# Kernel tuning notes

Hardware: AMD Instinct MI355X
Metric: run time of the kernel (lower is better)

The kernel has to match this reference:

```python
import jax, jax.numpy as jnp
import numpy as np

EMBED_DIM = 1024
NUM_HEADS = 16
HEAD_DIM = EMBED_DIM // NUM_HEADS
ROPE_BASE = 10000.0


def setup_inputs() -> dict:
    key = jax.random.key(0)
    ks = jax.random.split(key, 5)
    B, S, E = 4, 2048, EMBED_DIM
    hidden = jax.random.normal(ks[0], (B, S, E), dtype=jnp.float32)
    sc_in = 1.0 / np.sqrt(E)
    qkv_w = jax.random.normal(ks[1], (3 * E, E), dtype=jnp.float32) * sc_in
    qkv_b = jnp.zeros((3 * E,), dtype=jnp.float32)
    proj_w = jax.random.normal(ks[2], (E, E), dtype=jnp.float32) * sc_in
    proj_b = jnp.zeros((E,), dtype=jnp.float32)
    return {"hidden": hidden, "qkv_w": qkv_w, "qkv_b": qkv_b,
            "proj_w": proj_w, "proj_b": proj_b}


def _rope_cos_sin(position_ids, head_dim, base):
    # position_ids: [B, S] int; returns cos/sin of shape [B, 1, S, head_dim]
    inv_freq = 1.0 / (base ** (jnp.arange(0, head_dim, 2, dtype=jnp.float32) / head_dim))
    freqs = position_ids.astype(jnp.float32)[..., None] * inv_freq  # [B,S,hd/2]
    emb = jnp.concatenate([freqs, freqs], axis=-1)                  # [B,S,hd]
    return jnp.cos(emb)[:, None], jnp.sin(emb)[:, None]


def _rotate_half(x):
    x1, x2 = jnp.split(x, 2, axis=-1)
    return jnp.concatenate([-x2, x1], axis=-1)


def reference(hidden, qkv_w, qkv_b, proj_w, proj_b):
    B, S, E = hidden.shape
    H, hd = NUM_HEADS, HEAD_DIM
    qkv = hidden @ qkv_w.T + qkv_b                    # [B,S,3E]
    qkv = qkv.reshape(B, S, 3, H, hd).transpose(2, 0, 3, 1, 4)  # [3,B,H,S,hd]
    q, k, v = qkv[0], qkv[1], qkv[2]
    pos = jnp.broadcast_to(jnp.arange(S)[None, :], (B, S))
    cos, sin = _rope_cos_sin(pos, hd, ROPE_BASE)      # [B,1,S,hd]
    q = q * cos + _rotate_half(q) * sin
    k = k * cos + _rotate_half(k) * sin
    scale = 1.0 / jnp.sqrt(jnp.float32(hd))
    scores = jnp.einsum("bhsd,bhtd->bhst", q, k) * scale
    attn = jax.nn.softmax(scores, axis=-1)
    out = jnp.einsum("bhst,bhtd->bhsd", attn, v)      # [B,H,S,hd]
    out = out.transpose(0, 2, 1, 3).reshape(B, S, E)
    return out @ proj_w.T + proj_b
```

## Files before the change

kernel.cpp:

```cpp
#include <hip/hip_runtime.h>
#include <cstdint>
#include <cstddef>

typedef _Float16 f16;
typedef __attribute__((ext_vector_type(4))) float f32x4;
typedef __attribute__((ext_vector_type(8))) _Float16 f16x8;
typedef __attribute__((ext_vector_type(4))) _Float16 f16x4;

#define S_SEQ 2048
#define E_DIM 1024

#define OFF_HID   0ull
#define OFF_QKVW  8388608ull
#define OFF_PROJW 11534336ull
#define OFF_Q     12582912ull
#define OFF_K     20971520ull
#define OFF_VT    29360128ull
#define OFF_AO    37748736ull

__device__ __forceinline__ void async_copy16(const void* g, void* l) {
  __builtin_amdgcn_global_load_lds(
      (const __attribute__((address_space(1))) unsigned int*)g,
      (__attribute__((address_space(3))) unsigned int*)l, 16, 0, 0);
}

__device__ __forceinline__ float fast_exp2(float x) {
#if __has_builtin(__builtin_amdgcn_exp2f)
  return __builtin_amdgcn_exp2f(x);
#else
  return __expf(x * 0.6931471805599453f);
#endif
}

__global__ __launch_bounds__(256) void cvt_kernel(const float* __restrict__ hid,
                                                  const float* __restrict__ qw,
                                                  const float* __restrict__ pw,
                                                  f16* __restrict__ ws) {
  long i = (long)blockIdx.x * 256 + threadIdx.x;
  const float* src;
  f16* dst;
  long idx;
  if (i < 2097152L) { src = hid; dst = ws + OFF_HID;  idx = i; }
  else if (i < 2883584L) { src = qw; dst = ws + OFF_QKVW; idx = i - 2097152L; }
  else { src = pw; dst = ws + OFF_PROJW; idx = i - 2883584L; }
  float4 v = *(const float4*)(src + idx * 4);
  f16x4 o = { (f16)v.x, (f16)v.y, (f16)v.z, (f16)v.w };
  *(f16x4*)(dst + idx * 4) = o;
}

template <int MODE>
__global__ __launch_bounds__(256)
void gemm_kernel(const f16* __restrict__ A, const f16* __restrict__ Bm,
                 const float* __restrict__ bias,
                 f16* __restrict__ q_out, f16* __restrict__ k_out,
                 f16* __restrict__ vT_out, float* __restrict__ f_out) {
  __shared__ __align__(16) f16 As[2][128 * 32];
  __shared__ __align__(16) f16 Bs[2][128 * 32];
  const int tid = threadIdx.x;
  const int wave = tid >> 6;
  const int lane = tid & 63;
  const int q4 = lane >> 4;
  const int l16 = lane & 15;
  const int m0 = blockIdx.y * 128;
  const int n0 = blockIdx.x * 128;
  const int wr = (wave >> 1) * 64;
  const int wc = (wave & 1) * 64;
  f32x4 acc[4][4] = {};

  const int srow = tid >> 2;
  const int scol = (tid & 3) * 8;

  auto stage = [&](int k0, int b) {
    for (int p = 0; p < 2; ++p) {
      int row = p * 64 + srow;
      async_copy16(A + (size_t)(m0 + row) * 1024 + k0 + scol,
                   &As[b][(size_t)(p * 256 + wave * 64) * 8]);
      async_copy16(Bm + (size_t)(n0 + row) * 1024 + k0 + scol,
                   &Bs[b][(size_t)(p * 256 + wave * 64) * 8]);
    }
  };

  stage(0, 0);
  __syncthreads();
  int buf = 0;
  for (int k0 = 0; k0 < 1024; k0 += 32) {
    if (k0 + 32 < 1024) stage(k0 + 32, buf ^ 1);
    f16x8 af[4], bf[4];
    for (int mt = 0; mt < 4; ++mt)
      af[mt] = *(const f16x8*)&As[buf][(wr + mt * 16 + l16) * 32 + q4 * 8];
    for (int nt = 0; nt < 4; ++nt)
      bf[nt] = *(const f16x8*)&Bs[buf][(wc + nt * 16 + l16) * 32 + q4 * 8];
    for (int mt = 0; mt < 4; ++mt)
      for (int nt = 0; nt < 4; ++nt)
        acc[mt][nt] = __builtin_amdgcn_mfma_f32_16x16x32_f16(af[mt], bf[nt],
                                                             acc[mt][nt], 0, 0, 0);
    __syncthreads();
    buf ^= 1;
  }

  if constexpr (MODE == 0) {
    const int bx = blockIdx.x;
    const int part = bx >> 3;
    const int h = (((bx & 7) * 128) + wc) >> 6;
    float bv[4];
    for (int nt = 0; nt < 4; ++nt) bv[nt] = bias[n0 + wc + nt * 16 + l16];
    if (part < 2) {
      f16* outp = (part == 0) ? q_out : k_out;
      const float qscale = (part == 0) ? 0.18033688011112042f : 1.0f;
      float invf[2];
      for (int nt = 0; nt < 2; ++nt)
        invf[nt] = __expf(-(float)(nt * 16 + l16) * 0.2878231366242557f);
      for (int mt = 0; mt < 4; ++mt) {
        int mbase = m0 + wr + mt * 16 + q4 * 4;
        for (int r = 0; r < 4; ++r) {
          int mm = mbase + r;
          int b = mm >> 11, s = mm & 2047;
          size_t rowb = ((size_t)((b * 16 + h) * 2048 + s)) * 64;
          for (int nt = 0; nt < 2; ++nt) {
            float x1 = acc[mt][nt][r] + bv[nt];
            float x2 = acc[mt][nt + 2][r] + bv[nt + 2];
            float ang = (float)s * invf[nt];
            float sn, cs;
            __sincosf(ang, &sn, &cs);
            float o1 = (x1 * cs - x2 * sn) * qscale;
            float o2 = (x2 * cs + x1 * sn) * qscale;
            int d1 = nt * 16 + l16;
            outp[rowb + d1] = (f16)o1;
            outp[rowb + d1 + 32] = (f16)o2;
          }
        }
      }
    } else {
      for (int mt = 0; mt < 4; ++mt) {
        int mbase = m0 + wr + mt * 16 + q4 * 4;
        int b = mbase >> 11, s0 = mbase & 2047;
        for (int nt = 0; nt < 4; ++nt) {
          int d = nt * 16 + l16;
          size_t basei = ((size_t)((b * 16 + h) * 64 + d)) * 2048 + s0;
          f16x4 pk;
          for (int r = 0; r < 4; ++r) pk[r] = (f16)(acc[mt][nt][r] + bv[nt]);
          *(f16x4*)&vT_out[basei] = pk;
        }
      }
    }
  } else {
    float bv[4];
    for (int nt = 0; nt < 4; ++nt) bv[nt] = bias[n0 + wc + nt * 16 + l16];
    for (int mt = 0; mt < 4; ++mt)
      for (int r = 0; r < 4; ++r) {
        int mm = m0 + wr + mt * 16 + q4 * 4 + r;
        for (int nt = 0; nt < 4; ++nt)
          f_out[(size_t)mm * 1024 + n0 + wc + nt * 16 + l16] = acc[mt][nt][r] + bv[nt];
      }
  }
}

__global__ __launch_bounds__(256, 2)
void attn_kernel(const f16* __restrict__ Qg, const f16* __restrict__ Kg,
                 const f16* __restrict__ VTg, f16* __restrict__ AOg) {
  __shared__ __align__(16) f16 smem[2][8704];
  const int tid = threadIdx.x;
  const int wave = tid >> 6, lane = tid & 63;
  const int q4 = lane >> 4, l16 = lane & 15;
  const int qt = blockIdx.x, bh = blockIdx.y;
  const f16* Qb = Qg + (size_t)bh * (S_SEQ * 64);
  const f16* Kb = Kg + (size_t)bh * (S_SEQ * 64);
  const f16* Vb = VTg + (size_t)bh * (64 * S_SEQ);
  const int ws0 = wave * 64;

  f16x8 qf[4][2];
#pragma unroll
  for (int sn = 0; sn < 4; ++sn)
#pragma unroll
    for (int kf = 0; kf < 2; ++kf)
      qf[sn][kf] = *(const f16x8*)(Qb + (size_t)(qt * 256 + ws0 + sn * 16 + l16) * 64
                                      + kf * 32 + q4 * 8);

  f32x4 o[4][4] = {};
  f32x4 lacc[4] = {};
  f16x8 ones;
#pragma unroll
  for (int j = 0; j < 8; ++j) ones[j] = (f16)1.0f;

  const int srow = tid >> 3;
  const int scol = (tid & 7) * 8;

  const int kcs = scol >> 5;
  const int hs8 = ((scol >> 4) & 1) * 8;
  const int q0s = (scol & 15) >> 2;
  const int slot0 = kcs * 4 + q0s;
  const int swzA = (((slot0) ^ (srow & 7)) << 4) + hs8;
  const int swzB = (((slot0 + 1) ^ (srow & 7)) << 4) + hs8;

  int4 k0r = *(const int4*)(Kb + (size_t)srow * 64 + scol);
  int4 k1r = *(const int4*)(Kb + (size_t)(32 + srow) * 64 + scol);
  f16x8 v0r = *(const f16x8*)(Vb + (size_t)srow * 2048 + scol);
  f16x8 v1r = *(const f16x8*)(Vb + (size_t)(32 + srow) * 2048 + scol);
  {
    f16* Kn = smem[0];
    char* Vn = (char*)(smem[0] + 4608);
    *(int4*)(Kn + srow * 72 + scol) = k0r;
    *(int4*)(Kn + (32 + srow) * 72 + scol) = k1r;
    f16x4 lo0 = {v0r[0], v0r[1], v0r[2], v0r[3]};
    f16x4 hi0 = {v0r[4], v0r[5], v0r[6], v0r[7]};
    f16x4 lo1 = {v1r[0], v1r[1], v1r[2], v1r[3]};
    f16x4 hi1 = {v1r[4], v1r[5], v1r[6], v1r[7]};
    *(f16x4*)(Vn + srow * 128 + swzA) = lo0;
    *(f16x4*)(Vn + srow * 128 + swzB) = hi0;
    *(f16x4*)(Vn + (32 + srow) * 128 + swzA) = lo1;
    *(f16x4*)(Vn + (32 + srow) * 128 + swzB) = hi1;
  }
  __syncthreads();

  int cur = 0;
  for (int tt = 0; tt < 32; ++tt) {
    const f16* Kc = smem[cur];
    const char* Vc = (const char*)(smem[cur] + 4608);

    if (tt + 1 < 32) {
      const int t0n = (tt + 1) * 64;
      k0r = *(const int4*)(Kb + (size_t)(t0n + srow) * 64 + scol);
      k1r = *(const int4*)(Kb + (size_t)(t0n + 32 + srow) * 64 + scol);
      v0r = *(const f16x8*)(Vb + (size_t)srow * 2048 + t0n + scol);
      v1r = *(const f16x8*)(Vb + (size_t)(32 + srow) * 2048 + t0n + scol);
    }

    f16x8 kf0[4], kf1[4];
#pragma unroll
    for (int tm = 0; tm < 4; ++tm) {
      kf0[tm] = *(const f16x8*)(Kc + (tm * 16 + l16) * 72 + q4 * 8);
      kf1[tm] = *(const f16x8*)(Kc + (tm * 16 + l16) * 72 + 32 + q4 * 8);
    }
    f16x8 vf[4][2];
#pragma unroll
    for (int dm = 0; dm < 4; ++dm)
#pragma unroll
      for (int kc = 0; kc < 2; ++kc)
        vf[dm][kc] = *(const f16x8*)(Vc + (dm * 16 + l16) * 128 +
                                     (((kc * 4 + q4) ^ (l16 & 7)) << 4));

#pragma unroll
    for (int sn = 0; sn < 4; ++sn) {
      f32x4 st[4];
#pragma unroll
      for (int tm = 0; tm < 4; ++tm) {
        f32x4 c = {0.f, 0.f, 0.f, 0.f};
        c = __builtin_amdgcn_mfma_f32_16x16x32_f16(kf0[tm], qf[sn][0], c, 0, 0, 0);
        c = __builtin_amdgcn_mfma_f32_16x16x32_f16(kf1[tm], qf[sn][1], c, 0, 0, 0);
        st[tm] = c;
      }
#pragma unroll
      for (int tm = 0; tm < 4; ++tm)
#pragma unroll
        for (int r = 0; r < 4; ++r)
          st[tm][r] = fast_exp2(st[tm][r]);
#pragma unroll
      for (int kc = 0; kc < 2; ++kc) {
        f16x8 pf;
        pf[0] = (f16)st[kc * 2][0];
        pf[1] = (f16)st[kc * 2][1];
        pf[2] = (f16)st[kc * 2][2];
        pf[3] = (f16)st[kc * 2][3];
        pf[4] = (f16)st[kc * 2 + 1][0];
        pf[5] = (f16)st[kc * 2 + 1][1];
        pf[6] = (f16)st[kc * 2 + 1][2];
        pf[7] = (f16)st[kc * 2 + 1][3];
        lacc[sn] = __builtin_amdgcn_mfma_f32_16x16x32_f16(ones, pf, lacc[sn], 0, 0, 0);
#pragma unroll
        for (int dm = 0; dm < 4; ++dm)
          o[dm][sn] = __builtin_amdgcn_mfma_f32_16x16x32_f16(vf[dm][kc], pf,
                                                             o[dm][sn], 0, 0, 0);
      }
    }

    if (tt + 1 < 32) {
      f16* Kn = smem[cur ^ 1];
      char* Vn = (char*)(smem[cur ^ 1] + 4608);
      *(int4*)(Kn + srow * 72 + scol) = k0r;
      *(int4*)(Kn + (32 + srow) * 72 + scol) = k1r;
      f16x4 lo0 = {v0r[0], v0r[1], v0r[2], v0r[3]};
      f16x4 hi0 = {v0r[4], v0r[5], v0r[6], v0r[7]};
      f16x4 lo1 = {v1r[0], v1r[1], v1r[2], v1r[3]};
      f16x4 hi1 = {v1r[4], v1r[5], v1r[6], v1r[7]};
      *(f16x4*)(Vn + srow * 128 + swzA) = lo0;
      *(f16x4*)(Vn + srow * 128 + swzB) = hi0;
      *(f16x4*)(Vn + (32 + srow) * 128 + swzA) = lo1;
      *(f16x4*)(Vn + (32 + srow) * 128 + swzB) = hi1;
    }
    __syncthreads();
    cur ^= 1;
  }

  float inv_l[4];
#pragma unroll
  for (int sn = 0; sn < 4; ++sn) inv_l[sn] = 1.0f / lacc[sn][0];
  f16* Ot = smem[0];
#pragma unroll
  for (int sn = 0; sn < 4; ++sn) {
    int so = ws0 + sn * 16 + l16;
#pragma unroll
    for (int dm = 0; dm < 4; ++dm) {
      f16x4 w;
      w[0] = (f16)(o[dm][sn][0] * inv_l[sn]);
      w[1] = (f16)(o[dm][sn][1] * inv_l[sn]);
      w[2] = (f16)(o[dm][sn][2] * inv_l[sn]);
      w[3] = (f16)(o[dm][sn][3] * inv_l[sn]);
      *(f16x4*)(Ot + so * 64 + dm * 16 + q4 * 4) = w;
    }
  }
  __syncthreads();
  const int b = bh >> 4, h = bh & 15;
#pragma unroll
  for (int half = 0; half < 2; ++half) {
    const int sr = half * 128 + (tid >> 1), dh = (tid & 1) * 32;
    size_t gbase = ((size_t)(b * 2048 + qt * 256 + sr)) * 1024 + h * 64 + dh;
#pragma unroll
    for (int c = 0; c < 4; ++c) {
      f16x8 v = *(const f16x8*)(Ot + sr * 64 + dh + c * 8);
      *(f16x8*)(AOg + gbase + c * 8) = v;
    }
  }
}

extern "C" void kernel_launch(void* const* d_in, const int* in_sizes, int n_in,
                              void* d_out, int out_size, void* d_ws, size_t ws_size,
                              hipStream_t stream) {
  const float* hid   = (const float*)d_in[0];
  const float* qkvw  = (const float*)d_in[1];
  const float* qkvb  = (const float*)d_in[2];
  const float* projw = (const float*)d_in[3];
  const float* projb = (const float*)d_in[4];
  float* out = (float*)d_out;
  f16* ws = (f16*)d_ws;

  cvt_kernel<<<12288, 256, 0, stream>>>(hid, qkvw, projw, ws);
  gemm_kernel<0><<<dim3(24, 64), 256, 0, stream>>>(
      ws + OFF_HID, ws + OFF_QKVW, qkvb,
      ws + OFF_Q, ws + OFF_K, ws + OFF_VT, nullptr);
  attn_kernel<<<dim3(8, 64), 256, 0, stream>>>(
      ws + OFF_Q, ws + OFF_K, ws + OFF_VT, ws + OFF_AO);
  gemm_kernel<1><<<dim3(8, 64), 256, 0, stream>>>(
      ws + OFF_AO, ws + OFF_PROJW, projb,
      nullptr, nullptr, nullptr, out);
}
```

Before: 269.0 us.

## Triple-buffer GEMM LDS staging with XOR swizzle and explicit vmcnt waits

Moves the shared QKV/projection GEMM main loop from double to triple buffering, keeping two async global-to-LDS stages in flight and waiting with explicit vmcnt counts and raw s_barrier in place of __syncthreads. It also applies an XOR swizzle to the LDS column layout, both where data is written and where fragments are read, to cut bank conflicts on the f16x8 fragment loads. The intent is to hide global load latency behind MFMA work and reduce LDS stalls. The cost is 50% more LDS per block, which may lower occupancy, and more fragile hand-written synchronisation.

```diff
diff --git a/kernel.cpp b/kernel.cpp
--- a/kernel.cpp
+++ b/kernel.cpp
@@ -54,8 +54,8 @@
                  const float* __restrict__ bias,
                  f16* __restrict__ q_out, f16* __restrict__ k_out,
                  f16* __restrict__ vT_out, float* __restrict__ f_out) {
-  __shared__ __align__(16) f16 As[2][128 * 32];
-  __shared__ __align__(16) f16 Bs[2][128 * 32];
+  __shared__ __align__(16) f16 As[3][128 * 32];
+  __shared__ __align__(16) f16 Bs[3][128 * 32];
   const int tid = threadIdx.x;
   const int wave = tid >> 6;
   const int lane = tid & 63;
@@ -68,7 +68,7 @@
   f32x4 acc[4][4] = {};
 
   const int srow = tid >> 2;
-  const int scol = (tid & 3) * 8;
+  const int scol = (((tid & 3) ^ ((srow >> 2) & 3)) * 8);
 
   auto stage = [&](int k0, int b) {
     for (int p = 0; p < 2; ++p) {
@@ -80,23 +80,63 @@
     }
   };
 
+#define GEMM_STEP(cb, sb, ks, DO_STAGE, VMN)                                 \
+  {                                                                          \
+    if (DO_STAGE) stage(((ks) + 2) * 32, sb);                                \
+    f16x8 af[4], bf[4];                                                      \
+    _Pragma("unroll")                                                        \
+    for (int mt = 0; mt < 4; ++mt) {                                         \
+      int row = wr + mt * 16 + l16;                                          \
+      af[mt] = *(const f16x8*)&As[cb][row * 32 + (q4 ^ ((row >> 2) & 3)) * 8]; \
+    }                                                                        \
+    _Pragma("unroll")                                                        \
+    for (int nt = 0; nt < 4; ++nt) {                                         \
+      int row = wc + nt * 16 + l16;                                          \
+      bf[nt] = *(const f16x8*)&Bs[cb][row * 32 + (q4 ^ ((row >> 2) & 3)) * 8]; \
+    }                                                                        \
+    asm volatile("s_waitcnt lgkmcnt(0)" ::: "memory");                       \
+    __builtin_amdgcn_sched_barrier(0);                                       \
+    _Pragma("unroll")                                                        \
+    for (int mt = 0; mt < 4; ++mt)                                           \
+      _Pragma("unroll")                                                      \
+      for (int nt = 0; nt < 4; ++nt)                                         \
+        acc[mt][nt] = __builtin_amdgcn_mfma_f32_16x16x32_f16(                \
+            af[mt], bf[nt], acc[mt][nt], 0, 0, 0);                           \
+    asm volatile("s_waitcnt vmcnt(" #VMN ")" ::: "memory");                  \
+    __builtin_amdgcn_s_barrier();                                            \
+  }
+
   stage(0, 0);
-  __syncthreads();
-  int buf = 0;
-  for (int k0 = 0; k0 < 1024; k0 += 32) {
-    if (k0 + 32 < 1024) stage(k0 + 32, buf ^ 1);
+  stage(32, 1);
+  asm volatile("s_waitcnt vmcnt(4)" ::: "memory");
+  __builtin_amdgcn_s_barrier();
+
+  for (int k3 = 0; k3 < 30; k3 += 3) {
+    GEMM_STEP(0, 2, (k3 + 0), 1, 4);
+    GEMM_STEP(1, 0, (k3 + 1), 1, 4);
+    GEMM_STEP(2, 1, (k3 + 2), 1, 4);
+  }
+  GEMM_STEP(0, 0, 30, 0, 0);
+  {
     f16x8 af[4], bf[4];
+#pragma unroll
+    for (int mt = 0; mt < 4; ++mt) {
+      int row = wr + mt * 16 + l16;
+      af[mt] = *(const f16x8*)&As[1][row * 32 + (q4 ^ ((row >> 2) & 3)) * 8];
+    }
+#pragma unroll
+    for (int nt = 0; nt < 4; ++nt) {
+      int row = wc + nt * 16 + l16;
+      bf[nt] = *(const f16x8*)&Bs[1][row * 32 + (q4 ^ ((row >> 2) & 3)) * 8];
+    }
+#pragma unroll
     for (int mt = 0; mt < 4; ++mt)
-      af[mt] = *(const f16x8*)&As[buf][(wr + mt * 16 + l16) * 32 + q4 * 8];
-    for (int nt = 0; nt < 4; ++nt)
-      bf[nt] = *(const f16x8*)&Bs[buf][(wc + nt * 16 + l16) * 32 + q4 * 8];
-    for (int mt = 0; mt < 4; ++mt)
+#pragma unroll
       for (int nt = 0; nt < 4; ++nt)
         acc[mt][nt] = __builtin_amdgcn_mfma_f32_16x16x32_f16(af[mt], bf[nt],
                                                              acc[mt][nt], 0, 0, 0);
-    __syncthreads();
-    buf ^= 1;
-  }
+  }
+#undef GEMM_STEP
 
   if constexpr (MODE == 0) {
     const int bx = blockIdx.x;
```

After: 270.7 us. No clear change (+0.6%).

## Restructure GEMM main loop into split-K half phases with finer waitcnt pipelining

Applied to the files above, without the earlier changes.

The GEMM K-loop now works on 64-wide K tiles, each split into two 32-wide halves with their own double-buffered LDS slots. Each phase reads its fragments with inline ds_read_b128, issues the async global-to-LDS copy for the next tile's matching half, and waits on explicit vmcnt counters rather than draining all loads behind a full __syncthreads. MFMA bursts are wrapped in sched_barrier and s_setprio to keep them together and favour math issue. This aims to overlap global loads with compute more tightly, at the cost of doubled LDS use (lower occupancy) and fragile hand-managed waitcnt and barrier ordering.

```diff
diff --git a/kernel.cpp b/kernel.cpp
--- a/kernel.cpp
+++ b/kernel.cpp
@@ -22,6 +22,14 @@
   __builtin_amdgcn_global_load_lds(
       (const __attribute__((address_space(1))) unsigned int*)g,
       (__attribute__((address_space(3))) unsigned int*)l, 16, 0, 0);
+}
+
+__device__ __forceinline__ f16x8 lds_read_b128(const f16* p) {
+  f16x8 r;
+  const __attribute__((address_space(3))) f16* p3 =
+      (const __attribute__((address_space(3))) f16*)p;
+  asm volatile("ds_read_b128 %0, %1" : "=v"(r) : "v"(p3));
+  return r;
 }
 
 __device__ __forceinline__ float fast_exp2(float x) {
@@ -54,8 +62,8 @@
                  const float* __restrict__ bias,
                  f16* __restrict__ q_out, f16* __restrict__ k_out,
                  f16* __restrict__ vT_out, float* __restrict__ f_out) {
-  __shared__ __align__(16) f16 As[2][128 * 32];
-  __shared__ __align__(16) f16 Bs[2][128 * 32];
+  __shared__ __align__(16) f16 As[2][2][128 * 32];
+  __shared__ __align__(16) f16 Bs[2][2][128 * 32];
   const int tid = threadIdx.x;
   const int wave = tid >> 6;
   const int lane = tid & 63;
@@ -70,33 +78,54 @@
   const int srow = tid >> 2;
   const int scol = (tid & 3) * 8;
 
-  auto stage = [&](int k0, int b) {
-    for (int p = 0; p < 2; ++p) {
-      int row = p * 64 + srow;
-      async_copy16(A + (size_t)(m0 + row) * 1024 + k0 + scol,
-                   &As[b][(size_t)(p * 256 + wave * 64) * 8]);
-      async_copy16(Bm + (size_t)(n0 + row) * 1024 + k0 + scol,
-                   &Bs[b][(size_t)(p * 256 + wave * 64) * 8]);
-    }
+  auto stage = [&](int kt, int kh, int b) {
+    const f16* as = A + (size_t)(m0 + srow) * 1024 + kt * 64 + kh * 32 + scol;
+    async_copy16(as,             &As[b][kh][wave * 512]);
+    async_copy16(as + 64 * 1024, &As[b][kh][2048 + wave * 512]);
+    const f16* bs = Bm + (size_t)(n0 + srow) * 1024 + kt * 64 + kh * 32 + scol;
+    async_copy16(bs,             &Bs[b][kh][wave * 512]);
+    async_copy16(bs + 64 * 1024, &Bs[b][kh][2048 + wave * 512]);
   };
 
-  stage(0, 0);
-  __syncthreads();
-  int buf = 0;
-  for (int k0 = 0; k0 < 1024; k0 += 32) {
-    if (k0 + 32 < 1024) stage(k0 + 32, buf ^ 1);
-    f16x8 af[4], bf[4];
-    for (int mt = 0; mt < 4; ++mt)
-      af[mt] = *(const f16x8*)&As[buf][(wr + mt * 16 + l16) * 32 + q4 * 8];
-    for (int nt = 0; nt < 4; ++nt)
-      bf[nt] = *(const f16x8*)&Bs[buf][(wc + nt * 16 + l16) * 32 + q4 * 8];
-    for (int mt = 0; mt < 4; ++mt)
-      for (int nt = 0; nt < 4; ++nt)
-        acc[mt][nt] = __builtin_amdgcn_mfma_f32_16x16x32_f16(af[mt], bf[nt],
-                                                             acc[mt][nt], 0, 0, 0);
-    __syncthreads();
-    buf ^= 1;
-  }
+#define PHASE(T, KH, DO_STAGE, VMN)                                          \
+  {                                                                          \
+    const int cb_ = (T) & 1;                                                 \
+    f16x8 af[4], bf[4];                                                      \
+    _Pragma("unroll")                                                        \
+    for (int mt = 0; mt < 4; ++mt)                                           \
+      af[mt] = lds_read_b128(&As[cb_][KH][(wr + mt * 16 + l16) * 32 + q4 * 8]); \
+    _Pragma("unroll")                                                        \
+    for (int nt = 0; nt < 4; ++nt)                                           \
+      bf[nt] = lds_read_b128(&Bs[cb_][KH][(wc + nt * 16 + l16) * 32 + q4 * 8]); \
+    if (DO_STAGE) stage((T) + 1, KH, cb_ ^ 1);                               \
+    __builtin_amdgcn_s_barrier();                                            \
+    asm volatile("s_waitcnt lgkmcnt(0)" ::: "memory");                       \
+    __builtin_amdgcn_sched_barrier(0);                                       \
+    __builtin_amdgcn_s_setprio(1);                                           \
+    _Pragma("unroll")                                                        \
+    for (int mt = 0; mt < 4; ++mt)                                           \
+      _Pragma("unroll")                                                      \
+      for (int nt = 0; nt < 4; ++nt)                                         \
+        acc[mt][nt] = __builtin_amdgcn_mfma_f32_16x16x32_f16(                \
+            af[mt], bf[nt], acc[mt][nt], 0, 0, 0);                           \
+    __builtin_amdgcn_s_setprio(0);                                           \
+    __builtin_amdgcn_sched_barrier(0);                                       \
+    asm volatile("s_waitcnt vmcnt(" #VMN ")" ::: "memory");                  \
+    __builtin_amdgcn_s_barrier();                                            \
+  }
+
+  stage(0, 0, 0);
+  stage(0, 1, 0);
+  asm volatile("s_waitcnt vmcnt(4)" ::: "memory");
+  __builtin_amdgcn_s_barrier();
+
+  for (int t = 0; t < 15; ++t) {
+    PHASE(t, 0, 1, 4);
+    PHASE(t, 1, 1, 4);
+  }
+  PHASE(15, 0, 0, 0);
+  PHASE(15, 1, 0, 0);
+#undef PHASE
 
   if constexpr (MODE == 0) {
     const int bx = blockIdx.x;
```

New measurement: 268.1 us. About the same (-0.3%).

## Rewrite GEMM as 256x256 tile, 8-wave kernel with swizzled LDS and phased pipeline

Applied to the files above, without the earlier changes.

Rewrites the shared GEMM kernel so that 512 threads compute 256x256 output tiles with K-steps of 64. Global-to-LDS staging goes through XOR-swizzled async copies, and fragments are read with explicit ds_read_b128. The main loop is split into phases that interleave staging of the next tile with MFMA work under explicit barriers, waitcnt and setprio. The goal is more data reuse per loaded byte, fewer LDS bank conflicts and better overlap of loads with compute. In exchange the kernel needs much more register and LDS use, and the QKV GEMM launches only 384 blocks and the projection GEMM only 128, which can leave many of the chip's CUs idle.

```diff
diff --git a/kernel.cpp b/kernel.cpp
--- a/kernel.cpp
+++ b/kernel.cpp
@@ -22,6 +22,14 @@
   __builtin_amdgcn_global_load_lds(
       (const __attribute__((address_space(1))) unsigned int*)g,
       (__attribute__((address_space(3))) unsigned int*)l, 16, 0, 0);
+}
+
+__device__ __forceinline__ f16x8 lds_read_b128(const f16* p) {
+  f16x8 r;
+  const __attribute__((address_space(3))) f16* p3 =
+      (const __attribute__((address_space(3))) f16*)p;
+  asm volatile("ds_read_b128 %0, %1" : "=v"(r) : "v"(p3));
+  return r;
 }
 
 __device__ __forceinline__ float fast_exp2(float x) {
@@ -49,76 +57,129 @@
 }
 
 template <int MODE>
-__global__ __launch_bounds__(256)
+__global__ __launch_bounds__(512)
 void gemm_kernel(const f16* __restrict__ A, const f16* __restrict__ Bm,
                  const float* __restrict__ bias,
                  f16* __restrict__ q_out, f16* __restrict__ k_out,
                  f16* __restrict__ vT_out, float* __restrict__ f_out) {
-  __shared__ __align__(16) f16 As[2][128 * 32];
-  __shared__ __align__(16) f16 Bs[2][128 * 32];
+  __shared__ __align__(16) f16 As[2][2][8192];
+  __shared__ __align__(16) f16 Bs[2][2][8192];
   const int tid = threadIdx.x;
   const int wave = tid >> 6;
   const int lane = tid & 63;
   const int q4 = lane >> 4;
   const int l16 = lane & 15;
-  const int m0 = blockIdx.y * 128;
-  const int n0 = blockIdx.x * 128;
-  const int wr = (wave >> 1) * 64;
-  const int wc = (wave & 1) * 64;
-  f32x4 acc[4][4] = {};
-
-  const int srow = tid >> 2;
-  const int scol = (tid & 3) * 8;
-
-  auto stage = [&](int k0, int b) {
-    for (int p = 0; p < 2; ++p) {
-      int row = p * 64 + srow;
-      async_copy16(A + (size_t)(m0 + row) * 1024 + k0 + scol,
-                   &As[b][(size_t)(p * 256 + wave * 64) * 8]);
-      async_copy16(Bm + (size_t)(n0 + row) * 1024 + k0 + scol,
-                   &Bs[b][(size_t)(p * 256 + wave * 64) * 8]);
-    }
+  const int wm = wave >> 2;
+  const int wn = wave & 3;
+  const int m0 = blockIdx.y * 256;
+  const int n0 = blockIdx.x * 256;
+  f32x4 acc[8][4] = {};
+
+  const int gsl = ((lane & 3) ^ ((lane >> 2) & 3)) * 8;
+  const f16* Agp = A  + (size_t)(m0 + wave * 16 + (lane >> 2)) * 1024 + gsl;
+  const f16* Bgp = Bm + (size_t)(n0 + wave * 16 + (lane >> 2)) * 1024 + gsl;
+  char* AsW = (char*)&As[0][0][0] + wave * 1024;
+  char* BsW = (char*)&Bs[0][0][0] + wave * 1024;
+
+  auto stageA = [&](int kt, int kc, int sb) {
+    const f16* g = Agp + kt * 64 + kc * 32;
+    char* l = AsW + sb * 32768 + kc * 16384;
+    async_copy16(g, l);
+    async_copy16(g + 131072, l + 8192);
   };
-
-  stage(0, 0);
-  __syncthreads();
-  int buf = 0;
-  for (int k0 = 0; k0 < 1024; k0 += 32) {
-    if (k0 + 32 < 1024) stage(k0 + 32, buf ^ 1);
-    f16x8 af[4], bf[4];
-    for (int mt = 0; mt < 4; ++mt)
-      af[mt] = *(const f16x8*)&As[buf][(wr + mt * 16 + l16) * 32 + q4 * 8];
-    for (int nt = 0; nt < 4; ++nt)
-      bf[nt] = *(const f16x8*)&Bs[buf][(wc + nt * 16 + l16) * 32 + q4 * 8];
-    for (int mt = 0; mt < 4; ++mt)
-      for (int nt = 0; nt < 4; ++nt)
-        acc[mt][nt] = __builtin_amdgcn_mfma_f32_16x16x32_f16(af[mt], bf[nt],
-                                                             acc[mt][nt], 0, 0, 0);
-    __syncthreads();
-    buf ^= 1;
-  }
+  auto stageB = [&](int kt, int kc, int sb) {
+    const f16* g = Bgp + kt * 64 + kc * 32;
+    char* l = BsW + sb * 32768 + kc * 16384;
+    async_copy16(g, l);
+    async_copy16(g + 131072, l + 8192);
+  };
+
+  const int aoff = (wm * 128 + l16) * 32 + (q4 ^ (l16 & 3)) * 8;
+  const int boff = (wn * 64 + l16) * 32 + (q4 ^ (l16 & 3)) * 8;
+
+  f16x8 bf[4];
+
+#define PHASE(b_, kc_, mh_, STAGE_STMT, VM_STMT)                          \
+  do {                                                                    \
+    const f16* pA_ = &As[b_][kc_][0];                                     \
+    const f16* pB_ = &Bs[b_][kc_][0];                                     \
+    f16x8 af_[4];                                                         \
+    _Pragma("unroll")                                                     \
+    for (int i_ = 0; i_ < 4; ++i_)                                        \
+      af_[i_] = lds_read_b128(pA_ + aoff + (mh_) * 2048 + i_ * 512);      \
+    if ((mh_) == 0) {                                                     \
+      _Pragma("unroll")                                                   \
+      for (int nt_ = 0; nt_ < 4; ++nt_)                                   \
+        bf[nt_] = lds_read_b128(pB_ + boff + nt_ * 512);                  \
+    }                                                                     \
+    STAGE_STMT;                                                           \
+    __builtin_amdgcn_s_barrier();                                         \
+    asm volatile("s_waitcnt lgkmcnt(0)" ::: "memory");                    \
+    __builtin_amdgcn_sched_barrier(0);                                    \
+    __builtin_amdgcn_s_setprio(1);                                        \
+    _Pragma("unroll")                                                     \
+    for (int i_ = 0; i_ < 4; ++i_)                                        \
+      _Pragma("unroll")                                                   \
+      for (int nt_ = 0; nt_ < 4; ++nt_)                                   \
+        acc[(mh_) * 4 + i_][nt_] = __builtin_amdgcn_mfma_f32_16x16x32_f16(\
+            af_[i_], bf[nt_], acc[(mh_) * 4 + i_][nt_], 0, 0, 0);         \
+    __builtin_amdgcn_s_setprio(0);                                        \
+    VM_STMT;                                                              \
+    __builtin_amdgcn_s_barrier();                                         \
+  } while (0)
+
+#define VM4 asm volatile("s_waitcnt vmcnt(4)" ::: "memory")
+#define VM0 asm volatile("s_waitcnt vmcnt(0)" ::: "memory")
+
+#define KTILE(b_, t_)                                                     \
+  PHASE(b_, 0, 0, stageA((t_) + 1, 0, (b_) ^ 1), (void)0);                \
+  PHASE(b_, 0, 1, stageB((t_) + 1, 0, (b_) ^ 1), VM4);                    \
+  PHASE(b_, 1, 0, stageA((t_) + 1, 1, (b_) ^ 1), (void)0);                \
+  PHASE(b_, 1, 1, stageB((t_) + 1, 1, (b_) ^ 1), VM4)
+
+  stageA(0, 0, 0);
+  stageB(0, 0, 0);
+  stageA(0, 1, 0);
+  stageB(0, 1, 0);
+  VM4;
+  __builtin_amdgcn_s_barrier();
+
+  for (int t2 = 0; t2 < 14; t2 += 2) {
+    KTILE(0, t2);
+    KTILE(1, t2 + 1);
+  }
+  KTILE(0, 14);
+  PHASE(1, 0, 0, (void)0, (void)0);
+  PHASE(1, 0, 1, (void)0, VM0);
+  PHASE(1, 1, 0, (void)0, (void)0);
+  PHASE(1, 1, 1, (void)0, (void)0);
+
+#undef KTILE
+#undef VM4
+#undef VM0
+#undef PHASE
 
   if constexpr (MODE == 0) {
-    const int bx = blockIdx.x;
-    const int part = bx >> 3;
-    const int h = (((bx & 7) * 128) + wc) >> 6;
+    const int part = n0 >> 10;
+    const int colb = (n0 & 1023) + wn * 64;
+    const int h = colb >> 6;
     float bv[4];
-    for (int nt = 0; nt < 4; ++nt) bv[nt] = bias[n0 + wc + nt * 16 + l16];
+    for (int nt = 0; nt < 4; ++nt) bv[nt] = bias[n0 + wn * 64 + nt * 16 + l16];
     if (part < 2) {
       f16* outp = (part == 0) ? q_out : k_out;
       const float qscale = (part == 0) ? 0.18033688011112042f : 1.0f;
       float invf[2];
       for (int nt = 0; nt < 2; ++nt)
         invf[nt] = __expf(-(float)(nt * 16 + l16) * 0.2878231366242557f);
-      for (int mt = 0; mt < 4; ++mt) {
-        int mbase = m0 + wr + mt * 16 + q4 * 4;
+      for (int a = 0; a < 8; ++a) {
+        int mbase = m0 + wm * 128 + (a >> 2) * 64 + (a & 3) * 16 + q4 * 4;
         for (int r = 0; r < 4; ++r) {
           int mm = mbase + r;
           int b = mm >> 11, s = mm & 2047;
           size_t rowb = ((size_t)((b * 16 + h) * 2048 + s)) * 64;
           for (int nt = 0; nt < 2; ++nt) {
-            float x1 = acc[mt][nt][r] + bv[nt];
-            float x2 = acc[mt][nt + 2][r] + bv[nt + 2];
+            float x1 = acc[a][nt][r] + bv[nt];
+            float x2 = acc[a][nt + 2][r] + bv[nt + 2];
             float ang = (float)s * invf[nt];
             float sn, cs;
             __sincosf(ang, &sn, &cs);
@@ -131,26 +192,27 @@
         }
       }
     } else {
-      for (int mt = 0; mt < 4; ++mt) {
-        int mbase = m0 + wr + mt * 16 + q4 * 4;
+      for (int a = 0; a < 8; ++a) {
+        int mbase = m0 + wm * 128 + (a >> 2) * 64 + (a & 3) * 16 + q4 * 4;
         int b = mbase >> 11, s0 = mbase & 2047;
         for (int nt = 0; nt < 4; ++nt) {
           int d = nt * 16 + l16;
           size_t basei = ((size_t)((b * 16 + h) * 64 + d)) * 2048 + s0;
           f16x4 pk;
-          for (int r = 0; r < 4; ++r) pk[r] = (f16)(acc[mt][nt][r] + bv[nt]);
+          for (int r = 0; r < 4; ++r) pk[r] = (f16)(acc[a][nt][r] + bv[nt]);
           *(f16x4*)&vT_out[basei] = pk;
         }
       }
     }
   } else {
     float bv[4];
-    for (int nt = 0; nt < 4; ++nt) bv[nt] = bias[n0 + wc + nt * 16 + l16];
-    for (int mt = 0; mt < 4; ++mt)
+    for (int nt = 0; nt < 4; ++nt) bv[nt] = bias[n0 + wn * 64 + nt * 16 + l16];
+    for (int a = 0; a < 8; ++a)
       for (int r = 0; r < 4; ++r) {
-        int mm = m0 + wr + mt * 16 + q4 * 4 + r;
+        int mm = m0 + wm * 128 + (a >> 2) * 64 + (a & 3) * 16 + q4 * 4 + r;
         for (int nt = 0; nt < 4; ++nt)
-          f_out[(size_t)mm * 1024 + n0 + wc + nt * 16 + l16] = acc[mt][nt][r] + bv[nt];
+          f_out[(size_t)mm * 1024 + n0 + wn * 64 + nt * 16 + l16] =
+              acc[a][nt][r] + bv[nt];
       }
   }
 }
@@ -334,12 +396,12 @@
   f16* ws = (f16*)d_ws;
 
   cvt_kernel<<<12288, 256, 0, stream>>>(hid, qkvw, projw, ws);
-  gemm_kernel<0><<<dim3(24, 64), 256, 0, stream>>>(
+  gemm_kernel<0><<<dim3(12, 32), 512, 0, stream>>>(
       ws + OFF_HID, ws + OFF_QKVW, qkvb,
       ws + OFF_Q, ws + OFF_K, ws + OFF_VT, nullptr);
   attn_kernel<<<dim3(8, 64), 256, 0, stream>>>(
       ws + OFF_Q, ws + OFF_K, ws + OFF_VT, ws + OFF_AO);
-  gemm_kernel<1><<<dim3(8, 64), 256, 0, stream>>>(
+  gemm_kernel<1><<<dim3(4, 32), 512, 0, stream>>>(
       ws + OFF_AO, ws + OFF_PROJW, projb,
       nullptr, nullptr, nullptr, out);
 }
```

After: 277.3 us. 1.03x slower.
